# Kernel tuning notes

Hardware: AMD Instinct MI355X
Metric: run time of the kernel (lower is better)

Reference implementation:

```python
import jax, jax.numpy as jnp
import numpy as np

N = 262144
K = 1024
D = 256
DECAY = 0.99
EPS = 1e-5


def setup_inputs() -> dict:
    key = jax.random.key(0)
    k1, k2, k3, k4 = jax.random.split(key, 4)
    indices = jax.random.randint(k1, (N,), 0, K)
    encodings = jax.random.normal(k2, (N, D), dtype=jnp.float32)
    cluster_size = jax.random.uniform(k3, (K,), dtype=jnp.float32)
    embed_avg = jax.random.normal(k4, (K, D), dtype=jnp.float32)
    return {"indices": indices, "encodings": encodings,
            "cluster_size": cluster_size, "embed_avg": embed_avg}


def reference(indices, encodings, cluster_size, embed_avg):
    # indices: [N] int, encodings: [N, D], cluster_size: [K], embed_avg: [K, D]
    # Faithful to: one_hot.sum(0) and encodings.T @ one_hot == per-code scatter sums.
    idx = indices.reshape(-1)
    enc = encodings.reshape(-1, D)
    counts = jax.ops.segment_sum(jnp.ones((idx.shape[0],), enc.dtype), idx,
                                 num_segments=K)              # [K]
    embed_sum = jax.ops.segment_sum(enc, idx, num_segments=K)  # [K, D]
    new_cs = cluster_size * DECAY + (1.0 - DECAY) * counts
    new_ea = embed_avg * DECAY + (1.0 - DECAY) * embed_sum
    n = new_cs.sum()
    smoothed = (new_cs + EPS) / (n + K * EPS) * n
    embed_normalized = new_ea / smoothed[:, None]
    return new_cs, new_ea, embed_normalized
```

## Files before the change

### kernel.cpp

```cpp
#include <hip/hip_runtime.h>

#define N_TOT   262144
#define KCODES  1024
#define DIM     256
#define DECAY   0.99f
#define OMDECAY 0.01f
#define EPS     1e-5f

__global__ void k_hist(const int* __restrict__ idx, int* __restrict__ counts) {
    for (int i = blockIdx.x * blockDim.x + threadIdx.x; i < N_TOT;
         i += gridDim.x * blockDim.x) {
        atomicAdd(&counts[idx[i]], 1);
    }
}

__global__ void k_scan(const int* __restrict__ counts,
                       const float* __restrict__ cluster_size,
                       int* __restrict__ offsets,
                       int* __restrict__ cursor,
                       float* __restrict__ smoothed,
                       float* __restrict__ out_cs) {
    __shared__ int   sc[KCODES];
    __shared__ float sf[KCODES];
    const int t = threadIdx.x;

    const int c = counts[t];
    sc[t] = c;
    __syncthreads();
    for (int off = 1; off < KCODES; off <<= 1) {
        int v = (t >= off) ? sc[t - off] : 0;
        __syncthreads();
        sc[t] += v;
        __syncthreads();
    }
    const int excl = sc[t] - c;
    offsets[t] = excl;
    cursor[t]  = excl;

    const float ncs = cluster_size[t] * DECAY + OMDECAY * (float)c;
    out_cs[t] = ncs;
    sf[t] = ncs;
    __syncthreads();
    for (int off = KCODES / 2; off > 0; off >>= 1) {
        if (t < off) sf[t] += sf[t + off];
        __syncthreads();
    }
    const float n = sf[0];
    smoothed[t] = (ncs + EPS) / (n + (float)KCODES * EPS) * n;
}

__global__ void k_scatter(const int* __restrict__ idx,
                          int* __restrict__ cursor,
                          int* __restrict__ sorted) {
    for (int i = blockIdx.x * blockDim.x + threadIdx.x; i < N_TOT;
         i += gridDim.x * blockDim.x) {
        int pos = atomicAdd(&cursor[idx[i]], 1);
        sorted[pos] = i;
    }
}

__global__ void __launch_bounds__(DIM)
k_sum(const float* __restrict__ enc,
      const float* __restrict__ embed_avg,
      const int* __restrict__ counts,
      const int* __restrict__ offsets,
      const int* __restrict__ sorted,
      const float* __restrict__ smoothed,
      float* __restrict__ out) {
    const int k = blockIdx.x;
    const int t = threadIdx.x;
    const int start = offsets[k];
    const int cnt   = counts[k];

    float acc = 0.f;
    int j = 0;
    for (; j + 8 <= cnt; j += 8) {
        int r0 = sorted[start + j + 0];
        int r1 = sorted[start + j + 1];
        int r2 = sorted[start + j + 2];
        int r3 = sorted[start + j + 3];
        int r4 = sorted[start + j + 4];
        int r5 = sorted[start + j + 5];
        int r6 = sorted[start + j + 6];
        int r7 = sorted[start + j + 7];
        float a0 = enc[(size_t)r0 * DIM + t];
        float a1 = enc[(size_t)r1 * DIM + t];
        float a2 = enc[(size_t)r2 * DIM + t];
        float a3 = enc[(size_t)r3 * DIM + t];
        float a4 = enc[(size_t)r4 * DIM + t];
        float a5 = enc[(size_t)r5 * DIM + t];
        float a6 = enc[(size_t)r6 * DIM + t];
        float a7 = enc[(size_t)r7 * DIM + t];
        acc += a0; acc += a1; acc += a2; acc += a3;
        acc += a4; acc += a5; acc += a6; acc += a7;
    }
    for (; j < cnt; ++j) {
        int r = sorted[start + j];
        acc += enc[(size_t)r * DIM + t];
    }

    const float ea = embed_avg[(size_t)k * DIM + t] * DECAY + OMDECAY * acc;
    out[KCODES + (size_t)k * DIM + t] = ea;
    out[KCODES + (size_t)KCODES * DIM + (size_t)k * DIM + t] = ea / smoothed[k];
}

extern "C" void kernel_launch(void* const* d_in, const int* in_sizes, int n_in,
                              void* d_out, int out_size, void* d_ws, size_t ws_size,
                              hipStream_t stream) {
    const int*   idx = (const int*)  d_in[0];
    const float* enc = (const float*)d_in[1];
    const float* cs  = (const float*)d_in[2];
    const float* ea  = (const float*)d_in[3];
    float* out = (float*)d_out;

    char* ws = (char*)d_ws;
    int*   counts   = (int*)  (ws);
    int*   offsets  = (int*)  (ws + 1 * KCODES * 4);
    int*   cursor   = (int*)  (ws + 2 * KCODES * 4);
    float* smoothed = (float*)(ws + 3 * KCODES * 4);
    int*   sorted   = (int*)  (ws + 4 * KCODES * 4);

    hipMemsetAsync(counts, 0, KCODES * sizeof(int), stream);
    k_hist   <<<1024, 256, 0, stream>>>(idx, counts);
    k_scan   <<<1, KCODES, 0, stream>>>(counts, cs, offsets, cursor, smoothed, out);
    k_scatter<<<1024, 256, 0, stream>>>(idx, cursor, sorted);
    k_sum    <<<KCODES, DIM, 0, stream>>>(enc, ea, counts, offsets, sorted, smoothed, out);
}
```

Baseline: 483.8 us.

## Vectorize index and encoding loads, use wave-shuffle scan, split rows across waves

The histogram and scatter kernels now load indices as int4, with one thread per four indices and no grid-stride loop. The scan kernel swaps its shared-memory Hillis-Steele scan and tree reduction for wavefront shuffle scans, which cuts the number of block barriers. The sum kernel now reads encodings as float4. Each of the four waves takes every fourth row of a code, and the partial sums are combined through shared memory. Wider loads mean fewer memory instructions and more bytes in flight per gather, at the cost of an extra reduction step and a changed summation order.

```diff
diff --git a/kernel.cpp b/kernel.cpp
--- a/kernel.cpp
+++ b/kernel.cpp
@@ -7,11 +7,13 @@
 #define OMDECAY 0.01f
 #define EPS     1e-5f
 
-__global__ void k_hist(const int* __restrict__ idx, int* __restrict__ counts) {
-    for (int i = blockIdx.x * blockDim.x + threadIdx.x; i < N_TOT;
-         i += gridDim.x * blockDim.x) {
-        atomicAdd(&counts[idx[i]], 1);
-    }
+__global__ void k_hist(const int4* __restrict__ idx4, int* __restrict__ counts) {
+    int i = blockIdx.x * blockDim.x + threadIdx.x;
+    int4 v = idx4[i];
+    atomicAdd(&counts[v.x], 1);
+    atomicAdd(&counts[v.y], 1);
+    atomicAdd(&counts[v.z], 1);
+    atomicAdd(&counts[v.w], 1);
 }
 
 __global__ void k_scan(const int* __restrict__ counts,
@@ -20,88 +22,134 @@
                        int* __restrict__ cursor,
                        float* __restrict__ smoothed,
                        float* __restrict__ out_cs) {
-    __shared__ int   sc[KCODES];
-    __shared__ float sf[KCODES];
-    const int t = threadIdx.x;
+    __shared__ int   wsum[16];
+    __shared__ float wf[16];
+    __shared__ float n_sh;
+    const int t   = threadIdx.x;
+    const int wid = t >> 6;
+    const int l   = t & 63;
 
     const int c = counts[t];
-    sc[t] = c;
+    int v = c;
+    #pragma unroll
+    for (int d = 1; d < 64; d <<= 1) {
+        int u = __shfl_up(v, d, 64);
+        if (l >= d) v += u;
+    }
+    if (l == 63) wsum[wid] = v;
+
+    const float ncs = cluster_size[t] * DECAY + OMDECAY * (float)c;
+    out_cs[t] = ncs;
+    float fs = ncs;
+    #pragma unroll
+    for (int d = 32; d; d >>= 1) fs += __shfl_xor(fs, d, 64);
+    if (l == 0) wf[wid] = fs;
     __syncthreads();
-    for (int off = 1; off < KCODES; off <<= 1) {
-        int v = (t >= off) ? sc[t - off] : 0;
-        __syncthreads();
-        sc[t] += v;
-        __syncthreads();
+
+    if (wid == 0) {
+        int s = (l < 16) ? wsum[l] : 0;
+        #pragma unroll
+        for (int d = 1; d < 16; d <<= 1) {
+            int u = __shfl_up(s, d, 64);
+            if (l >= d) s += u;
+        }
+        if (l < 16) wsum[l] = s;
+        float x = (l < 16) ? wf[l] : 0.f;
+        #pragma unroll
+        for (int d = 8; d; d >>= 1) x += __shfl_xor(x, d, 16);
+        if (l == 0) n_sh = x;
     }
-    const int excl = sc[t] - c;
+    __syncthreads();
+
+    const int wbase = wid ? wsum[wid - 1] : 0;
+    const int excl  = v + wbase - c;
     offsets[t] = excl;
     cursor[t]  = excl;
 
-    const float ncs = cluster_size[t] * DECAY + OMDECAY * (float)c;
-    out_cs[t] = ncs;
-    sf[t] = ncs;
-    __syncthreads();
-    for (int off = KCODES / 2; off > 0; off >>= 1) {
-        if (t < off) sf[t] += sf[t + off];
-        __syncthreads();
-    }
-    const float n = sf[0];
+    const float n = n_sh;
     smoothed[t] = (ncs + EPS) / (n + (float)KCODES * EPS) * n;
 }
 
-__global__ void k_scatter(const int* __restrict__ idx,
+__global__ void k_scatter(const int4* __restrict__ idx4,
                           int* __restrict__ cursor,
                           int* __restrict__ sorted) {
-    for (int i = blockIdx.x * blockDim.x + threadIdx.x; i < N_TOT;
-         i += gridDim.x * blockDim.x) {
-        int pos = atomicAdd(&cursor[idx[i]], 1);
-        sorted[pos] = i;
-    }
+    int i = blockIdx.x * blockDim.x + threadIdx.x;
+    int4 v = idx4[i];
+    int b = i * 4;
+    sorted[atomicAdd(&cursor[v.x], 1)] = b;
+    sorted[atomicAdd(&cursor[v.y], 1)] = b + 1;
+    sorted[atomicAdd(&cursor[v.z], 1)] = b + 2;
+    sorted[atomicAdd(&cursor[v.w], 1)] = b + 3;
 }
 
-__global__ void __launch_bounds__(DIM)
-k_sum(const float* __restrict__ enc,
-      const float* __restrict__ embed_avg,
+__global__ void __launch_bounds__(256)
+k_sum(const float4* __restrict__ enc4,
+      const float4* __restrict__ ea4,
       const int* __restrict__ counts,
       const int* __restrict__ offsets,
       const int* __restrict__ sorted,
       const float* __restrict__ smoothed,
-      float* __restrict__ out) {
+      float4* __restrict__ out4) {
     const int k = blockIdx.x;
     const int t = threadIdx.x;
+    const int w = t >> 6;
+    const int l = t & 63;
     const int start = offsets[k];
     const int cnt   = counts[k];
 
-    float acc = 0.f;
-    int j = 0;
-    for (; j + 8 <= cnt; j += 8) {
-        int r0 = sorted[start + j + 0];
-        int r1 = sorted[start + j + 1];
-        int r2 = sorted[start + j + 2];
-        int r3 = sorted[start + j + 3];
-        int r4 = sorted[start + j + 4];
-        int r5 = sorted[start + j + 5];
-        int r6 = sorted[start + j + 6];
-        int r7 = sorted[start + j + 7];
-        float a0 = enc[(size_t)r0 * DIM + t];
-        float a1 = enc[(size_t)r1 * DIM + t];
-        float a2 = enc[(size_t)r2 * DIM + t];
-        float a3 = enc[(size_t)r3 * DIM + t];
-        float a4 = enc[(size_t)r4 * DIM + t];
-        float a5 = enc[(size_t)r5 * DIM + t];
-        float a6 = enc[(size_t)r6 * DIM + t];
-        float a7 = enc[(size_t)r7 * DIM + t];
-        acc += a0; acc += a1; acc += a2; acc += a3;
-        acc += a4; acc += a5; acc += a6; acc += a7;
+    float4 acc = make_float4(0.f, 0.f, 0.f, 0.f);
+    int j = w;
+    for (; j + 28 < cnt; j += 32) {
+        int r0 = sorted[start + j];
+        int r1 = sorted[start + j + 4];
+        int r2 = sorted[start + j + 8];
+        int r3 = sorted[start + j + 12];
+        int r4 = sorted[start + j + 16];
+        int r5 = sorted[start + j + 20];
+        int r6 = sorted[start + j + 24];
+        int r7 = sorted[start + j + 28];
+        float4 a0 = enc4[(size_t)r0 * 64 + l];
+        float4 a1 = enc4[(size_t)r1 * 64 + l];
+        float4 a2 = enc4[(size_t)r2 * 64 + l];
+        float4 a3 = enc4[(size_t)r3 * 64 + l];
+        float4 a4 = enc4[(size_t)r4 * 64 + l];
+        float4 a5 = enc4[(size_t)r5 * 64 + l];
+        float4 a6 = enc4[(size_t)r6 * 64 + l];
+        float4 a7 = enc4[(size_t)r7 * 64 + l];
+        acc.x += a0.x + a1.x + a2.x + a3.x + a4.x + a5.x + a6.x + a7.x;
+        acc.y += a0.y + a1.y + a2.y + a3.y + a4.y + a5.y + a6.y + a7.y;
+        acc.z += a0.z + a1.z + a2.z + a3.z + a4.z + a5.z + a6.z + a7.z;
+        acc.w += a0.w + a1.w + a2.w + a3.w + a4.w + a5.w + a6.w + a7.w;
     }
-    for (; j < cnt; ++j) {
+    for (; j < cnt; j += 4) {
         int r = sorted[start + j];
-        acc += enc[(size_t)r * DIM + t];
+        float4 a = enc4[(size_t)r * 64 + l];
+        acc.x += a.x; acc.y += a.y; acc.z += a.z; acc.w += a.w;
     }
 
-    const float ea = embed_avg[(size_t)k * DIM + t] * DECAY + OMDECAY * acc;
-    out[KCODES + (size_t)k * DIM + t] = ea;
-    out[KCODES + (size_t)KCODES * DIM + (size_t)k * DIM + t] = ea / smoothed[k];
+    __shared__ float4 red[3][64];
+    if (w > 0) red[w - 1][l] = acc;
+    __syncthreads();
+    if (w == 0) {
+        float4 p0 = red[0][l], p1 = red[1][l], p2 = red[2][l];
+        acc.x += p0.x + p1.x + p2.x;
+        acc.y += p0.y + p1.y + p2.y;
+        acc.z += p0.z + p1.z + p2.z;
+        acc.w += p0.w + p1.w + p2.w;
+
+        float4 ea = ea4[(size_t)k * 64 + l];
+        float4 nea;
+        nea.x = ea.x * DECAY + OMDECAY * acc.x;
+        nea.y = ea.y * DECAY + OMDECAY * acc.y;
+        nea.z = ea.z * DECAY + OMDECAY * acc.z;
+        nea.w = ea.w * DECAY + OMDECAY * acc.w;
+        out4[KCODES / 4 + (size_t)k * 64 + l] = nea;
+
+        const float s = smoothed[k];
+        float4 nrm;
+        nrm.x = nea.x / s; nrm.y = nea.y / s; nrm.z = nea.z / s; nrm.w = nea.w / s;
+        out4[KCODES / 4 + (size_t)KCODES * 64 + (size_t)k * 64 + l] = nrm;
+    }
 }
 
 extern "C" void kernel_launch(void* const* d_in, const int* in_sizes, int n_in,
@@ -121,8 +169,10 @@
     int*   sorted   = (int*)  (ws + 4 * KCODES * 4);
 
     hipMemsetAsync(counts, 0, KCODES * sizeof(int), stream);
-    k_hist   <<<1024, 256, 0, stream>>>(idx, counts);
+    k_hist   <<<N_TOT / 4 / 256, 256, 0, stream>>>((const int4*)idx, counts);
     k_scan   <<<1, KCODES, 0, stream>>>(counts, cs, offsets, cursor, smoothed, out);
-    k_scatter<<<1024, 256, 0, stream>>>(idx, cursor, sorted);
-    k_sum    <<<KCODES, DIM, 0, stream>>>(enc, ea, counts, offsets, sorted, smoothed, out);
+    k_scatter<<<N_TOT / 4 / 256, 256, 0, stream>>>((const int4*)idx, cursor, sorted);
+    k_sum    <<<KCODES, 256, 0, stream>>>((const float4*)enc, (const float4*)ea,
+                                          counts, offsets, sorted, smoothed,
+                                          (float4*)out);
 }
```

Result: slower. 497.9 us (+2.9%).
